# Kernel tuning notes

Measured on AMD Instinct MI355X. Metric: run time of the kernel, lower is better.

Reference implementation:

```python
import jax, jax.numpy as jnp
import numpy as np

GROUP_SIZE = 64  # quantization group size along in_features (K)


def setup_inputs() -> dict:
    key = jax.random.key(0)
    k1, k2, k3, k4, k5 = jax.random.split(key, 5)
    M, K, N = 32, 8192, 8192
    num_groups = K // GROUP_SIZE
    x = jax.random.normal(k1, (M, K), dtype=jnp.float32)
    # packed int4 weights: two nibbles per byte along K -> [N, K//2]
    packed_weight = jax.random.randint(k2, (N, K // 2), 0, 256, dtype=jnp.int32)
    scales = jax.random.uniform(k3, (N, num_groups), dtype=jnp.float32) * 0.02 + 1e-3
    zeros = jax.random.uniform(k4, (N, num_groups), dtype=jnp.float32) * 15.0
    bias_param = jax.random.normal(k5, (N,), dtype=jnp.float32)
    return {"x": x, "packed_weight": packed_weight, "scales": scales,
            "zeros": zeros, "bias_param": bias_param}


def reference(x, packed_weight, scales, zeros, bias_param):
    # x: [M, K] float; packed_weight: [N, K//2] int (uint8 semantics)
    # scales/zeros: [N, num_groups]; bias_param: [N]
    K = x.shape[-1]
    k = jnp.arange(K)
    shift = (k % 2) * 4                     # low nibble for even k, high for odd
    # unpack int4: q[n, k] in [0, 15]
    q = (packed_weight[:, k // 2] >> shift[None, :]) & 15   # [N, K]
    gidx = k // GROUP_SIZE                                  # [K]
    # group-wise dequant: (q - zero) * scale
    w = (q.astype(jnp.float32) - zeros[:, gidx]) * scales[:, gidx]  # [N, K]
    out = jnp.einsum('mk,nk->mn', x, w) + bias_param[None, :]        # [M, N]
    return out
```

## Files before the change

### kernel.cpp

```cpp
#include <hip/hip_runtime.h>
#include <hip/hip_bf16.h>
#include <stdint.h>


#define KK 8192
#define NN 8192
#define KP 4096
#define NG 128
#define BN 16
#define KSW 64
#define NKS 256
#define SCK 8
#define NSC 8
#define PWBUF 8192
#define KSPLIT 2

typedef __attribute__((ext_vector_type(8))) short short8;
typedef __attribute__((ext_vector_type(4))) float floatx4;
typedef const __attribute__((address_space(1))) void* gbl_t;
typedef __attribute__((address_space(3))) void* lds_t;

__device__ __forceinline__ void async16(const void* g, void* l) {
    __builtin_amdgcn_global_load_lds((gbl_t)(uintptr_t)g, (lds_t)(uintptr_t)l, 16, 0, 0);
}

__device__ __forceinline__ unsigned pack_bf16x2(float lo, float hi) {
    union { __hip_bfloat162 h; unsigned u; } c;
    c.h = __float22bfloat162_rn(make_float2(lo, hi));
    return c.u;
}

__device__ __forceinline__ unsigned dq2(int q, float sc, float zs) {
    float lo = fmaf((float)(q & 15),        sc, zs);
    float hi = fmaf((float)((q >> 4) & 15), sc, zs);
    unsigned ua = __float_as_uint(lo); ua += 0x7fffu + ((ua >> 16) & 1u);
    unsigned ub = __float_as_uint(hi); ub += 0x7fffu + ((ub >> 16) & 1u);
    return __builtin_amdgcn_perm(ub, ua, 0x07060302);
}

__global__ void prep_kernel(const float* __restrict__ x, const float* __restrict__ bias,
                            ushort* __restrict__ xb, float* __restrict__ out,
                            int xconv_blocks)
{
    const int bx = blockIdx.x;
    if (bx < xconv_blocks) {
        const int tid = bx * 256 + threadIdx.x;
        const int l   = tid & 63;
        const int ks  = (tid >> 6) & 255;
        const int mt  = tid >> 14;
        const int m   = (l & 15) + 16 * mt;
        const int kb  = ks * 32 + (l >> 4) * 8;
        const float* src = x + (size_t)m * KK + kb;
        const float4 a = *(const float4*)(src);
        const float4 b = *(const float4*)(src + 4);
        *(uint4*)(xb + (size_t)tid * 8) =
            make_uint4(pack_bf16x2(a.x, a.y), pack_bf16x2(a.z, a.w),
                       pack_bf16x2(b.x, b.y), pack_bf16x2(b.z, b.w));
    } else {
        const int f4 = (bx - xconv_blocks) * 256 + threadIdx.x;
        const int n4 = f4 & (NN / 4 - 1);
        ((float4*)out)[f4] = ((const float4*)bias)[n4];
    }
}

__global__ __launch_bounds__(256, 2)
void gptq_mfma_main(const int*   __restrict__ pw,
                    const float* __restrict__ scales,
                    const float* __restrict__ zeros,
                    const float* __restrict__ bias,
                    const ushort* __restrict__ xb,
                    float* __restrict__ out)
{
    __shared__ uint4 smem4[65536 / 16];
    uint8_t* smem = (uint8_t*)smem4;

    const int tid  = threadIdx.x;
    const int lane = tid & 63;
    const int wave = tid >> 6;
    const int n0   = blockIdx.x * BN;
    const int nl   = lane & 15;
    const int kq   = lane >> 4;
    const int ks0  = wave * KSW;

    float scr[32], zsr[32];
    {
        const float* sp = scales + (size_t)(n0 + nl) * NG + wave * 32;
        const float* zp = zeros  + (size_t)(n0 + nl) * NG + wave * 32;
#pragma unroll
        for (int i = 0; i < 8; ++i) {
            const float4 s4 = *(const float4*)(sp + i * 4);
            const float4 z4 = *(const float4*)(zp + i * 4);
            scr[i*4+0] = s4.x; zsr[i*4+0] = -z4.x * s4.x;
            scr[i*4+1] = s4.y; zsr[i*4+1] = -z4.y * s4.y;
            scr[i*4+2] = s4.z; zsr[i*4+2] = -z4.z * s4.z;
            scr[i*4+3] = s4.w; zsr[i*4+3] = -z4.w * s4.w;
        }
    }

    const int hw = lane >> 5, h = lane & 31, js = h >> 2, q = h & 3;
    int bofs[8];
#pragma unroll
    for (int i = 0; i < 8; ++i) {
        const int r  = 2 * i + hw;
        const int jg = js ^ (r & 7);
        const int qg = q ^ (i & 3);
        bofs[i] = (n0 + r) * KP + jg * 16 + qg * 4;
    }
    uint8_t* wbuf = smem + wave * (2 * PWBUF);
    const int pwo = (nl >> 1) * 1024 + (nl & 1) * 512 + ((kq ^ ((nl >> 1) & 3)) * 16);
    const int jx  = nl & 7;

#define STAGE(s) do {                                                  \
        uint8_t* b_ = wbuf + ((s) & 1) * PWBUF;                        \
        const int kb16_ = (ks0 + (s) * SCK) * 16;                      \
        _Pragma("unroll")                                              \
        for (int i_ = 0; i_ < 8; ++i_)                                 \
            async16(pw + bofs[i_] + kb16_, b_ + i_ * 1024);            \
    } while (0)

    const uint4* xfp = (const uint4*)xb;
    floatx4 acc0 = {0.f, 0.f, 0.f, 0.f};
    floatx4 acc1 = {0.f, 0.f, 0.f, 0.f};

    STAGE(0);

#pragma unroll
    for (int s = 0; s < NSC; ++s) {
        if (s + 1 < NSC) {
            STAGE(s + 1);
            asm volatile("s_waitcnt vmcnt(8)" ::: "memory");
        } else {
            asm volatile("s_waitcnt vmcnt(0)" ::: "memory");
        }
        uint8_t* b = wbuf + (s & 1) * PWBUF;
#pragma unroll
        for (int j = 0; j < SCK; ++j) {
            const int ks = ks0 + s * SCK + j;
            const int4 p = *(const int4*)(b + pwo + ((j ^ jx) * 64));
            union { uint4 v; short8 sv; } a0, a1, bf;
            a0.v = xfp[(size_t)(0 * NKS + ks) * 64 + lane];
            a1.v = xfp[(size_t)(1 * NKS + ks) * 64 + lane];
            const float sc = scr[s * 4 + (j >> 1)];
            const float zs = zsr[s * 4 + (j >> 1)];
            bf.v.x = dq2(p.x, sc, zs);
            bf.v.y = dq2(p.y, sc, zs);
            bf.v.z = dq2(p.z, sc, zs);
            bf.v.w = dq2(p.w, sc, zs);
            acc0 = __builtin_amdgcn_mfma_f32_16x16x32_bf16(a0.sv, bf.sv, acc0, 0, 0, 0);
            acc1 = __builtin_amdgcn_mfma_f32_16x16x32_bf16(a1.sv, bf.sv, acc1, 0, 0, 0);
        }
    }
#undef STAGE

    __syncthreads();
    float* red = (float*)smem;
#pragma unroll
    for (int r = 0; r < 4; ++r) {
        const int row = kq * 4 + r;
        red[(wave * 2 + 0) * 256 + row * 16 + nl] = acc0[r];
        red[(wave * 2 + 1) * 256 + row * 16 + nl] = acc1[r];
    }
    __syncthreads();

#pragma unroll
    for (int i = 0; i < 2; ++i) {
        const int e   = i * 256 + tid;
        const int mt  = e >> 8;
        const int idx = e & 255;
        const float sv = red[(0 * 2 + mt) * 256 + idx] + red[(1 * 2 + mt) * 256 + idx]
                       + red[(2 * 2 + mt) * 256 + idx] + red[(3 * 2 + mt) * 256 + idx];
        const int n = n0 + (idx & 15);
        out[(size_t)(mt * 16 + (idx >> 4)) * NN + n] = sv + bias[n];
    }
}

__global__ __launch_bounds__(256, 4)
void gptq_mfma_fallback(const int*   __restrict__ pw,
                        const float* __restrict__ scales,
                        const float* __restrict__ zeros,
                        const float* __restrict__ x,
                        float* __restrict__ out)
{
    __shared__ float s_lds[64][BN + 1];
    __shared__ float z_lds[64][BN + 1];
    __shared__ float red[4][2][256];

    const int tid  = threadIdx.x;
    const int lane = tid & 63;
    const int wave = tid >> 6;
    const int kh   = blockIdx.x & (KSPLIT - 1);
    const int n0   = (blockIdx.x >> 1) * BN;
    const int g0   = kh * 64;

    {
        const int r  = tid >> 4;
        const int gb = (tid & 15) * 4;
        const float4 s4 = *(const float4*)(scales + (size_t)(n0 + r) * NG + g0 + gb);
        const float4 z4 = *(const float4*)(zeros  + (size_t)(n0 + r) * NG + g0 + gb);
        s_lds[gb + 0][r] = s4.x; s_lds[gb + 1][r] = s4.y;
        s_lds[gb + 2][r] = s4.z; s_lds[gb + 3][r] = s4.w;
        z_lds[gb + 0][r] = z4.x; z_lds[gb + 1][r] = z4.y;
        z_lds[gb + 2][r] = z4.z; z_lds[gb + 3][r] = z4.w;
    }
    __syncthreads();

    const int nl = lane & 15;
    const int kq = lane >> 4;
    const int* pwp = pw + (size_t)(n0 + nl) * KP + kq * 4;
    const int ks0 = kh * 128 + wave * 32;

    auto load_xfrag = [&](int mt, int ks) -> uint4 {
        const float* src = x + (size_t)(nl + 16 * mt) * KK + ks * 32 + kq * 8;
        const float4 a = *(const float4*)(src);
        const float4 b = *(const float4*)(src + 4);
        return make_uint4(pack_bf16x2(a.x, a.y), pack_bf16x2(a.z, a.w),
                          pack_bf16x2(b.x, b.y), pack_bf16x2(b.z, b.w));
    };

    floatx4 acc0 = {0.f, 0.f, 0.f, 0.f};
    floatx4 acc1 = {0.f, 0.f, 0.f, 0.f};
    int4  pwb[4];
    uint4 x0b[4], x1b[4];

#pragma unroll
    for (int i = 0; i < 3; ++i) {
        const int ks = ks0 + i;
        pwb[i] = *(const int4*)(pwp + ks * 16);
        x0b[i] = load_xfrag(0, ks);
        x1b[i] = load_xfrag(1, ks);
    }

#pragma unroll 4
    for (int i = 0; i < 32; ++i) {
        const int slot = i & 3;
        if (i + 3 < 32) {
            const int ks = ks0 + i + 3;
            const int ps = (i + 3) & 3;
            pwb[ps] = *(const int4*)(pwp + ks * 16);
            x0b[ps] = load_xfrag(0, ks);
            x1b[ps] = load_xfrag(1, ks);
        }
        const int gl  = (wave * 32 + i) >> 1;
        const float sc = s_lds[gl][nl];
        const float zs = -z_lds[gl][nl] * sc;

        union { uint4 v; short8 sv; } bf, a0, a1;
        const int4 p = pwb[slot];
        bf.v.x = dq2(p.x, sc, zs);
        bf.v.y = dq2(p.y, sc, zs);
        bf.v.z = dq2(p.z, sc, zs);
        bf.v.w = dq2(p.w, sc, zs);
        a0.v = x0b[slot];
        a1.v = x1b[slot];
        acc0 = __builtin_amdgcn_mfma_f32_16x16x32_bf16(a0.sv, bf.sv, acc0, 0, 0, 0);
        acc1 = __builtin_amdgcn_mfma_f32_16x16x32_bf16(a1.sv, bf.sv, acc1, 0, 0, 0);
    }

#pragma unroll
    for (int r = 0; r < 4; ++r) {
        const int row = kq * 4 + r;
        red[wave][0][row * 16 + nl] = acc0[r];
        red[wave][1][row * 16 + nl] = acc1[r];
    }
    __syncthreads();

#pragma unroll
    for (int i = 0; i < 2; ++i) {
        const int e   = i * 256 + tid;
        const int mt  = e >> 8;
        const int idx = e & 255;
        const float s = red[0][mt][idx] + red[1][mt][idx] + red[2][mt][idx] + red[3][mt][idx];
        atomicAdd(out + (size_t)(mt * 16 + (idx >> 4)) * NN + n0 + (idx & 15), s);
    }
}

extern "C" void kernel_launch(void* const* d_in, const int* in_sizes, int n_in,
                              void* d_out, int out_size, void* d_ws, size_t ws_size,
                              hipStream_t stream) {
    const float* x      = (const float*)d_in[0];
    const int*   pw     = (const int*)  d_in[1];
    const float* scales = (const float*)d_in[2];
    const float* zeros  = (const float*)d_in[3];
    const float* bias   = (const float*)d_in[4];
    float* out = (float*)d_out;

    const size_t need = (size_t)32768 * 16;
    if (d_ws != nullptr && ws_size >= need) {
        ushort* xb = (ushort*)d_ws;
        prep_kernel<<<128, 256, 0, stream>>>(x, bias, xb, out, 128);
        gptq_mfma_main<<<NN / BN, 256, 0, stream>>>(pw, scales, zeros, bias, xb, out);
    } else {
        prep_kernel<<<256, 256, 0, stream>>>(x, bias, nullptr, out, 0);
        gptq_mfma_fallback<<<512 * KSPLIT, 256, 0, stream>>>(pw, scales, zeros, x, out);
    }
}
```

Measured before the change: 209.9 us.

## Replace LDS async weight staging with register-prefetched nontemporal global loads

The main kernel no longer stages packed weights through a double-buffered, swizzled LDS buffer using global_load_lds. Instead each lane loads its weight fragment directly into registers with a 3-deep software prefetch ring, using nontemporal loads, and outputs are written with nontemporal stores. This removes LDS staging traffic and the 64KB shared allocation, which may raise occupancy. The cost is more register pressure and less explicit control over in-flight memory requests. The fallback kernel also switches to nontemporal weight loads.

```diff
diff --git a/kernel.cpp b/kernel.cpp
--- a/kernel.cpp
+++ b/kernel.cpp
@@ -10,19 +10,11 @@
 #define BN 16
 #define KSW 64
 #define NKS 256
-#define SCK 8
-#define NSC 8
-#define PWBUF 8192
 #define KSPLIT 2
 
 typedef __attribute__((ext_vector_type(8))) short short8;
 typedef __attribute__((ext_vector_type(4))) float floatx4;
-typedef const __attribute__((address_space(1))) void* gbl_t;
-typedef __attribute__((address_space(3))) void* lds_t;
-
-__device__ __forceinline__ void async16(const void* g, void* l) {
-    __builtin_amdgcn_global_load_lds((gbl_t)(uintptr_t)g, (lds_t)(uintptr_t)l, 16, 0, 0);
-}
+typedef __attribute__((ext_vector_type(4))) int int4v;
 
 __device__ __forceinline__ unsigned pack_bf16x2(float lo, float hi) {
     union { __hip_bfloat162 h; unsigned u; } c;
@@ -71,8 +63,7 @@
                     const ushort* __restrict__ xb,
                     float* __restrict__ out)
 {
-    __shared__ uint4 smem4[65536 / 16];
-    uint8_t* smem = (uint8_t*)smem4;
+    __shared__ float red[4][2][256];
 
     const int tid  = threadIdx.x;
     const int lane = tid & 63;
@@ -97,68 +88,53 @@
         }
     }
 
-    const int hw = lane >> 5, h = lane & 31, js = h >> 2, q = h & 3;
-    int bofs[8];
-#pragma unroll
-    for (int i = 0; i < 8; ++i) {
-        const int r  = 2 * i + hw;
-        const int jg = js ^ (r & 7);
-        const int qg = q ^ (i & 3);
-        bofs[i] = (n0 + r) * KP + jg * 16 + qg * 4;
-    }
-    uint8_t* wbuf = smem + wave * (2 * PWBUF);
-    const int pwo = (nl >> 1) * 1024 + (nl & 1) * 512 + ((kq ^ ((nl >> 1) & 3)) * 16);
-    const int jx  = nl & 7;
-
-#define STAGE(s) do {                                                  \
-        uint8_t* b_ = wbuf + ((s) & 1) * PWBUF;                        \
-        const int kb16_ = (ks0 + (s) * SCK) * 16;                      \
-        _Pragma("unroll")                                              \
-        for (int i_ = 0; i_ < 8; ++i_)                                 \
-            async16(pw + bofs[i_] + kb16_, b_ + i_ * 1024);            \
-    } while (0)
-
+    const int* pwp = pw + (size_t)(n0 + nl) * KP + kq * 4;
     const uint4* xfp = (const uint4*)xb;
+
     floatx4 acc0 = {0.f, 0.f, 0.f, 0.f};
     floatx4 acc1 = {0.f, 0.f, 0.f, 0.f};
 
-    STAGE(0);
-
-#pragma unroll
-    for (int s = 0; s < NSC; ++s) {
-        if (s + 1 < NSC) {
-            STAGE(s + 1);
-            asm volatile("s_waitcnt vmcnt(8)" ::: "memory");
-        } else {
-            asm volatile("s_waitcnt vmcnt(0)" ::: "memory");
+    int4v pwb[4];
+    uint4 x0b[4], x1b[4];
+
+#pragma unroll
+    for (int i = 0; i < 3; ++i) {
+        const int ks = ks0 + i;
+        pwb[i] = __builtin_nontemporal_load((const int4v*)(pwp + ks * 16));
+        x0b[i] = xfp[(size_t)(0 * NKS + ks) * 64 + lane];
+        x1b[i] = xfp[(size_t)(1 * NKS + ks) * 64 + lane];
+    }
+
+#pragma unroll 4
+    for (int i = 0; i < KSW; ++i) {
+        const int slot = i & 3;
+        if (i + 3 < KSW) {
+            const int ks = ks0 + i + 3;
+            const int ps = (i + 3) & 3;
+            pwb[ps] = __builtin_nontemporal_load((const int4v*)(pwp + ks * 16));
+            x0b[ps] = xfp[(size_t)(0 * NKS + ks) * 64 + lane];
+            x1b[ps] = xfp[(size_t)(1 * NKS + ks) * 64 + lane];
         }
-        uint8_t* b = wbuf + (s & 1) * PWBUF;
-#pragma unroll
-        for (int j = 0; j < SCK; ++j) {
-            const int ks = ks0 + s * SCK + j;
-            const int4 p = *(const int4*)(b + pwo + ((j ^ jx) * 64));
-            union { uint4 v; short8 sv; } a0, a1, bf;
-            a0.v = xfp[(size_t)(0 * NKS + ks) * 64 + lane];
-            a1.v = xfp[(size_t)(1 * NKS + ks) * 64 + lane];
-            const float sc = scr[s * 4 + (j >> 1)];
-            const float zs = zsr[s * 4 + (j >> 1)];
-            bf.v.x = dq2(p.x, sc, zs);
-            bf.v.y = dq2(p.y, sc, zs);
-            bf.v.z = dq2(p.z, sc, zs);
-            bf.v.w = dq2(p.w, sc, zs);
-            acc0 = __builtin_amdgcn_mfma_f32_16x16x32_bf16(a0.sv, bf.sv, acc0, 0, 0, 0);
-            acc1 = __builtin_amdgcn_mfma_f32_16x16x32_bf16(a1.sv, bf.sv, acc1, 0, 0, 0);
-        }
-    }
-#undef STAGE
-
-    __syncthreads();
-    float* red = (float*)smem;
+        const float sc = scr[i >> 1];
+        const float zs = zsr[i >> 1];
+
+        union { uint4 v; short8 sv; } bf, a0, a1;
+        const int4v p = pwb[slot];
+        bf.v.x = dq2(p.x, sc, zs);
+        bf.v.y = dq2(p.y, sc, zs);
+        bf.v.z = dq2(p.z, sc, zs);
+        bf.v.w = dq2(p.w, sc, zs);
+        a0.v = x0b[slot];
+        a1.v = x1b[slot];
+        acc0 = __builtin_amdgcn_mfma_f32_16x16x32_bf16(a0.sv, bf.sv, acc0, 0, 0, 0);
+        acc1 = __builtin_amdgcn_mfma_f32_16x16x32_bf16(a1.sv, bf.sv, acc1, 0, 0, 0);
+    }
+
 #pragma unroll
     for (int r = 0; r < 4; ++r) {
         const int row = kq * 4 + r;
-        red[(wave * 2 + 0) * 256 + row * 16 + nl] = acc0[r];
-        red[(wave * 2 + 1) * 256 + row * 16 + nl] = acc1[r];
+        red[wave][0][row * 16 + nl] = acc0[r];
+        red[wave][1][row * 16 + nl] = acc1[r];
     }
     __syncthreads();
 
@@ -167,10 +143,11 @@
         const int e   = i * 256 + tid;
         const int mt  = e >> 8;
         const int idx = e & 255;
-        const float sv = red[(0 * 2 + mt) * 256 + idx] + red[(1 * 2 + mt) * 256 + idx]
-                       + red[(2 * 2 + mt) * 256 + idx] + red[(3 * 2 + mt) * 256 + idx];
+        const float sv = red[0][mt][idx] + red[1][mt][idx]
+                       + red[2][mt][idx] + red[3][mt][idx];
         const int n = n0 + (idx & 15);
-        out[(size_t)(mt * 16 + (idx >> 4)) * NN + n] = sv + bias[n];
+        __builtin_nontemporal_store(sv + bias[n],
+            out + (size_t)(mt * 16 + (idx >> 4)) * NN + n);
     }
 }
 
@@ -219,13 +196,13 @@
 
     floatx4 acc0 = {0.f, 0.f, 0.f, 0.f};
     floatx4 acc1 = {0.f, 0.f, 0.f, 0.f};
-    int4  pwb[4];
+    int4v pwb[4];
     uint4 x0b[4], x1b[4];
 
 #pragma unroll
     for (int i = 0; i < 3; ++i) {
         const int ks = ks0 + i;
-        pwb[i] = *(const int4*)(pwp + ks * 16);
+        pwb[i] = __builtin_nontemporal_load((const int4v*)(pwp + ks * 16));
         x0b[i] = load_xfrag(0, ks);
         x1b[i] = load_xfrag(1, ks);
     }
@@ -236,7 +213,7 @@
         if (i + 3 < 32) {
             const int ks = ks0 + i + 3;
             const int ps = (i + 3) & 3;
-            pwb[ps] = *(const int4*)(pwp + ks * 16);
+            pwb[ps] = __builtin_nontemporal_load((const int4v*)(pwp + ks * 16));
             x0b[ps] = load_xfrag(0, ks);
             x1b[ps] = load_xfrag(1, ks);
         }
@@ -245,7 +222,7 @@
         const float zs = -z_lds[gl][nl] * sc;
 
         union { uint4 v; short8 sv; } bf, a0, a1;
-        const int4 p = pwb[slot];
+        const int4v p = pwb[slot];
         bf.v.x = dq2(p.x, sc, zs);
         bf.v.y = dq2(p.y, sc, zs);
         bf.v.z = dq2(p.z, sc, zs);
```

New measurement: 223.7 us. 1.07x slower.
